# Kernel tuning notes

Measured on AMD Instinct MI355X. Metric: run time of the kernel, lower is better.

Reference implementation:

```python
import jax, jax.numpy as jnp
import numpy as np

B, PS, ENC = 64, 14, 2048
DEC, ATT, EMB = 512, 512, 512
V, L = 10000, 52


def setup_inputs() -> dict:
    key = jax.random.key(0)
    ks = jax.random.split(key, 24)
    rn = lambda k, shp, s=0.02: (jax.random.normal(k, shp) * s).astype(jnp.float32)
    lengths = jax.random.randint(ks[2], (B, 1), 2, L + 1)
    lengths = lengths.at[0, 0].set(L)  # ensure max(decode_lengths) == L-1 (static)
    return {
        "encoder_output": jax.random.normal(ks[0], (B, PS, PS, ENC), jnp.float32),
        "encoded_captions": jax.random.randint(ks[1], (B, L), 0, V),
        "caption_lengths": lengths,
        # embedding (torch init: uniform(-0.1, 0.1))
        "emb_W": jax.random.uniform(ks[3], (V, EMB), jnp.float32, -0.1, 0.1),
        # attention linears
        "att_enc_W": rn(ks[4], (ENC, ATT)), "att_enc_b": jnp.zeros((ATT,), jnp.float32),
        "att_dec_W": rn(ks[5], (DEC, ATT)), "att_dec_b": jnp.zeros((ATT,), jnp.float32),
        "att_full_w": rn(ks[6], (ATT,)), "att_full_b": jnp.zeros((), jnp.float32),
        # LSTMCell(input = EMB + ENC, hidden = DEC)
        "lstm_Wih": rn(ks[7], (4 * DEC, EMB + ENC)), "lstm_Whh": rn(ks[8], (4 * DEC, DEC)),
        "lstm_bih": jnp.zeros((4 * DEC,), jnp.float32), "lstm_bhh": jnp.zeros((4 * DEC,), jnp.float32),
        # init_h / init_c / f_beta / fc
        "initH_W": rn(ks[9], (ENC, DEC)), "initH_b": jnp.zeros((DEC,), jnp.float32),
        "initC_W": rn(ks[10], (ENC, DEC)), "initC_b": jnp.zeros((DEC,), jnp.float32),
        "fbeta_W": rn(ks[11], (DEC, ENC)), "fbeta_b": jnp.zeros((ENC,), jnp.float32),
        "fc_W": jax.random.uniform(ks[12], (DEC, V), jnp.float32, -0.1, 0.1),
        "fc_b": jnp.zeros((V,), jnp.float32),
    }


def reference(encoder_output, encoded_captions, caption_lengths,
              emb_W, att_enc_W, att_enc_b, att_dec_W, att_dec_b,
              att_full_w, att_full_b, lstm_Wih, lstm_Whh, lstm_bih, lstm_bhh,
              initH_W, initH_b, initC_W, initC_b, fbeta_W, fbeta_b, fc_W, fc_b):
    b = encoder_output.shape[0]
    lengths = caption_lengths[:, 0]
    order = jnp.argsort(-lengths)                     # sort descending (sort_idx)
    lengths = lengths[order]
    enc = encoder_output.reshape(b, -1, ENC)[order]   # [B, P, ENC]
    caps = encoded_captions[order]                    # [B, L]
    emb = emb_W[caps]                                 # [B, L, EMB]
    dec_len = lengths - 1                             # decode lengths
    T = caps.shape[1] - 1                             # static max(decode_lengths)

    mean_enc = enc.mean(axis=1)
    h0 = mean_enc @ initH_W + initH_b
    c0 = mean_enc @ initC_W + initC_b
    # precompute encoder half of the attention MLP once
    att1 = jnp.einsum('bpe,ea->bpa', enc, att_enc_W) + att_enc_b  # [B, P, ATT]

    def step(carry, t):
        h, c = carry
        mask = (t < dec_len)[:, None]                 # rows still decoding
        att2 = h @ att_dec_W + att_dec_b              # [B, ATT]
        e = jax.nn.relu(att1 + att2[:, None, :]) @ att_full_w + att_full_b  # [B, P]
        alpha = jax.nn.softmax(e, axis=-1)
        awe = jnp.einsum('bp,bpe->be', alpha, enc)    # attention-weighted encoding
        gate = jax.nn.sigmoid(h @ fbeta_W + fbeta_b)
        x = jnp.concatenate([emb[:, t, :], gate * awe], axis=1)
        gates = x @ lstm_Wih.T + lstm_bih + h @ lstm_Whh.T + lstm_bhh
        i, f, g, o = jnp.split(gates, 4, axis=1)
        c_new = jax.nn.sigmoid(f) * c + jax.nn.sigmoid(i) * jnp.tanh(g)
        h_new = jax.nn.sigmoid(o) * jnp.tanh(c_new)
        pred = h_new @ fc_W + fc_b                    # dropout p=0 -> identity
        h = jnp.where(mask, h_new, h)
        c = jnp.where(mask, c_new, c)
        return (h, c), (jnp.where(mask, pred, 0.0), jnp.where(mask, alpha, 0.0))

    _, (preds, alphas) = jax.lax.scan(step, (h0, c0), jnp.arange(T))
    preds = jnp.transpose(preds, (1, 0, 2))           # [B, T, V]
    alphas = jnp.transpose(alphas, (1, 0, 2))         # [B, T, P]
    return preds, caps, dec_len, alphas, order
```

## Files before the change

### kernel.cpp

```cpp
#include <hip/hip_runtime.h>
#include <hip/hip_cooperative_groups.h>
#include <math.h>

namespace cg = cooperative_groups;

#define BATCH 64
#define PIX   196
#define ENCD  2048
#define DECD  512
#define ATTD  512
#define EMBD  512
#define VOC   10000
#define LCAP  52
#define TSTEPS 51
#define XHDIM 3072

typedef __bf16 bfv8 __attribute__((ext_vector_type(8)));
typedef float  fv4  __attribute__((ext_vector_type(4)));

__device__ __forceinline__ float bf2f(unsigned short u) {
    union { unsigned int i; float f; } x; x.i = ((unsigned int)u) << 16; return x.f;
}
__device__ __forceinline__ unsigned short f2bf(float f) {
    union { float f; unsigned int i; } x; x.f = f;
    unsigned int r = x.i + 0x7fffu + ((x.i >> 16) & 1u);
    return (unsigned short)(r >> 16);
}

__global__ void k_setup(const int* caps, const int* lens,
                        int* order, int* declen,
                        float* caps_out, float* declen_out, float* order_out) {
    __shared__ int sl[64];
    __shared__ int so[64];
    int tid = threadIdx.x;
    sl[tid] = lens[tid];
    __syncthreads();
    int li = sl[tid];
    int pos = 0;
    for (int j = 0; j < 64; ++j) {
        int lj = sl[j];
        if (lj > li || (lj == li && j < tid)) pos++;
    }
    so[pos] = tid;
    __syncthreads();
    int ob = so[tid];
    order[tid] = ob;
    int dl = sl[ob] - 1;
    declen[tid] = dl;
    order_out[tid] = (float)ob;
    declen_out[tid] = (float)dl;
    for (int l = 0; l < LCAP; ++l)
        caps_out[tid * LCAP + l] = (float)caps[ob * LCAP + l];
}

__global__ void k_emb_all(const float* embW, const int* caps, const int* order,
                          unsigned short* emb_all, unsigned short* xh) {
    int b = blockIdx.x, t = blockIdx.y, tid = threadIdx.x;
    int tok = caps[order[b] * LCAP + t];
    float4 v = *(const float4*)(embW + (size_t)tok * EMBD + tid * 4);
    ushort4 o;
    o.x = f2bf(v.x); o.y = f2bf(v.y); o.z = f2bf(v.z); o.w = f2bf(v.w);
    *(ushort4*)(emb_all + ((size_t)t * 64 + b) * EMBD + tid * 4) = o;
    if (t == 0)
        *(ushort4*)(xh + (size_t)b * XHDIM + tid * 4) = o;
}

__global__ __launch_bounds__(256) void k_cvt_T(const float* src, unsigned short* dst,
                                               int R, int C) {
    __shared__ float tile[64][65];
    int c0 = blockIdx.x * 64, r0 = blockIdx.y * 64, tid = threadIdx.x;
    for (int idx = tid; idx < 4096; idx += 256) {
        int r = idx >> 6, c = idx & 63;
        float v = 0.f;
        if (r0 + r < R && c0 + c < C) v = src[(size_t)(r0 + r) * C + c0 + c];
        tile[r][c] = v;
    }
    __syncthreads();
    for (int idx = tid; idx < 4096; idx += 256) {
        int c = idx >> 6, r = idx & 63;
        if (c0 + c < C && r0 + r < R)
            dst[(size_t)(c0 + c) * R + r0 + r] = f2bf(tile[r][c]);
    }
}

__global__ void k_cvt_comb(const float* Wih, const float* Whh, unsigned short* W) {
    int j = blockIdx.x, tid = threadIdx.x;
    for (int k = tid * 4; k < XHDIM; k += 1024) {
        const float* src = (k < 2560) ? (Wih + (size_t)j * 2560 + k)
                                      : (Whh + (size_t)j * 512 + (k - 2560));
        float4 v = *(const float4*)src;
        ushort4 o;
        o.x = f2bf(v.x); o.y = f2bf(v.y); o.z = f2bf(v.z); o.w = f2bf(v.w);
        *(ushort4*)(W + (size_t)j * XHDIM + k) = o;
    }
}

__global__ void k_cvt_enc(const float* enc, const int* order, unsigned short* enc_bf) {
    int b = blockIdx.x, p = blockIdx.y, tid = threadIdx.x;
    const float* src = enc + ((size_t)order[b] * PIX + p) * ENCD + tid * 8;
    float4 v0 = *(const float4*)src;
    float4 v1 = *(const float4*)(src + 4);
    unsigned short o[8];
    o[0] = f2bf(v0.x); o[1] = f2bf(v0.y); o[2] = f2bf(v0.z); o[3] = f2bf(v0.w);
    o[4] = f2bf(v1.x); o[5] = f2bf(v1.y); o[6] = f2bf(v1.z); o[7] = f2bf(v1.w);
    *(uint4*)(enc_bf + ((size_t)b * PIX + p) * ENCD + tid * 8) = *(uint4*)o;
}

__global__ void k_mean(const float* enc, const int* order, float* meanv) {
    int b = blockIdx.x;
    int col = blockIdx.y * 256 + threadIdx.x;
    int ob = order[b];
    const float* base = enc + (size_t)ob * PIX * ENCD + col;
    float acc = 0.f;
    for (int p = 0; p < PIX; ++p) acc += base[(size_t)p * ENCD];
    meanv[b * ENCD + col] = acc * (1.0f / (float)PIX);
}

__global__ __launch_bounds__(256) void k_h0c0(const float* meanv,
                                              const float* WH, const float* bH,
                                              const float* WC, const float* bC,
                                              float* h, float* c, unsigned short* xh) {
    __shared__ float As[64 * 33];
    __shared__ float Bs[32 * 65];
    int nt = blockIdx.x, tid = threadIdx.x;
    const float* W; const float* bias; float* out; int j0; bool isH;
    if (nt < 8) { W = WH; bias = bH; out = h; j0 = nt * 64; isH = true; }
    else        { W = WC; bias = bC; out = c; j0 = (nt - 8) * 64; isH = false; }
    float acc[4][4] = {};
    int tr = tid & 15, tc = tid >> 4;
    for (int k0 = 0; k0 < ENCD; k0 += 32) {
        for (int idx = tid; idx < 512; idx += 256) {
            int rl = idx >> 3, k4 = (idx & 7) << 2;
            float4 v = *(const float4*)(meanv + (size_t)rl * ENCD + k0 + k4);
            float* d = As + rl * 33 + k4;
            d[0] = v.x; d[1] = v.y; d[2] = v.z; d[3] = v.w;
        }
        for (int idx = tid; idx < 512; idx += 256) {
            int k = idx >> 4, j4 = (idx & 15) << 2;
            float4 v = *(const float4*)(W + (size_t)(k0 + k) * DECD + j0 + j4);
            float* d = Bs + k * 65 + j4;
            d[0] = v.x; d[1] = v.y; d[2] = v.z; d[3] = v.w;
        }
        __syncthreads();
        for (int kk = 0; kk < 32; ++kk) {
            float a[4], bb[4];
            for (int i = 0; i < 4; ++i) a[i] = As[(tr * 4 + i) * 33 + kk];
            for (int i = 0; i < 4; ++i) bb[i] = Bs[kk * 65 + tc * 4 + i];
            for (int i = 0; i < 4; ++i)
                for (int j2 = 0; j2 < 4; ++j2) acc[i][j2] += a[i] * bb[j2];
        }
        __syncthreads();
    }
    for (int i = 0; i < 4; ++i)
        for (int j2 = 0; j2 < 4; ++j2) {
            int r = tr * 4 + i, j = j0 + tc * 4 + j2;
            float v = acc[i][j2] + bias[j];
            out[r * DECD + j] = v;
            if (isH) xh[(size_t)r * XHDIM + 2560 + j] = f2bf(v);
        }
}

__device__ __forceinline__ void mm64_core(
    const unsigned short* __restrict__ A, int lda,
    const unsigned short* __restrict__ Bt, int ldb,
    int K, int nvalid,
    unsigned short* __restrict__ As, unsigned short* __restrict__ Bs,
    fv4* __restrict__ acc)
{
    const int tid = threadIdx.x;
    const int lane = tid & 63;
    const int w = tid >> 6, wr = w >> 1, wc = w & 1;
    const int lr = lane & 15, lk = (lane >> 4) << 3;
    const int sr = tid >> 2, sc = (tid & 3) << 3;
    const unsigned short* ap = A + (size_t)sr * lda + sc;
    const unsigned short* bp = Bt + (size_t)sr * ldb + sc;
    const bool bok = sr < nvalid;
    unsigned short* aw = As + sr * 40 + sc;
    unsigned short* bw = Bs + sr * 40 + sc;
    const unsigned short* a0p = As + (wr * 32 + lr) * 40 + lk;
    const unsigned short* a1p = a0p + 16 * 40;
    const unsigned short* b0p = Bs + (wc * 32 + lr) * 40 + lk;
    const unsigned short* b1p = b0p + 16 * 40;

    uint4 av = *(const uint4*)ap;
    uint4 bv;
    if (bok) bv = *(const uint4*)bp; else { bv.x = bv.y = bv.z = bv.w = 0u; }

    for (int k0 = 0; k0 < K; k0 += 32) {
        __syncthreads();
        *(uint4*)aw = av;
        *(uint4*)bw = bv;
        if (k0 + 32 < K) {
            av = *(const uint4*)(ap + k0 + 32);
            if (bok) bv = *(const uint4*)(bp + k0 + 32);
            else { bv.x = bv.y = bv.z = bv.w = 0u; }
        }
        __syncthreads();
        bfv8 a0 = *(const bfv8*)a0p;
        bfv8 a1 = *(const bfv8*)a1p;
        bfv8 b0 = *(const bfv8*)b0p;
        bfv8 b1 = *(const bfv8*)b1p;
        acc[0] = __builtin_amdgcn_mfma_f32_16x16x32_bf16(a0, b0, acc[0], 0, 0, 0);
        acc[1] = __builtin_amdgcn_mfma_f32_16x16x32_bf16(a0, b1, acc[1], 0, 0, 0);
        acc[2] = __builtin_amdgcn_mfma_f32_16x16x32_bf16(a1, b0, acc[2], 0, 0, 0);
        acc[3] = __builtin_amdgcn_mfma_f32_16x16x32_bf16(a1, b1, acc[3], 0, 0, 0);
    }
}

#define MM64_DECL_EPI \
    int lane = threadIdx.x & 63; int w = threadIdx.x >> 6; \
    int wr = w >> 1, wc = w & 1; \
    int rg = (lane >> 4) << 2, cg = lane & 15;

__global__ __launch_bounds__(256) void k_att1_mfma(
    const unsigned short* __restrict__ enc_bf, const unsigned short* __restrict__ WaeT,
    const float* __restrict__ bias, unsigned short* __restrict__ att1bf) {
    __shared__ __align__(16) unsigned short As[64 * 40];
    __shared__ __align__(16) unsigned short Bs[64 * 40];
    int r0 = blockIdx.x * 64, a0 = blockIdx.y * 64;
    fv4 acc[4];
    acc[0] = (fv4)0.f; acc[1] = (fv4)0.f; acc[2] = (fv4)0.f; acc[3] = (fv4)0.f;
    mm64_core(enc_bf + (size_t)r0 * ENCD, ENCD,
              WaeT + (size_t)a0 * ENCD, ENCD, ENCD, 64, As, Bs, acc);
    MM64_DECL_EPI
    #pragma unroll
    for (int m = 0; m < 2; ++m)
      #pragma unroll
      for (int n = 0; n < 2; ++n)
        #pragma unroll
        for (int r = 0; r < 4; ++r) {
            int row = r0 + wr * 32 + m * 16 + rg + r;
            int col = a0 + wc * 32 + n * 16 + cg;
            att1bf[(size_t)row * ATTD + col] = f2bf(acc[m * 2 + n][r] + bias[col]);
        }
}

__global__ __launch_bounds__(256) void k_fc_mfma(
    const unsigned short* __restrict__ hallbf, const unsigned short* __restrict__ WfcT,
    const float* __restrict__ bias, const int* __restrict__ declen,
    float* __restrict__ preds) {
    __shared__ __align__(16) unsigned short As[64 * 40];
    __shared__ __align__(16) unsigned short Bs[64 * 40];
    int v0 = blockIdx.x * 64, tt = blockIdx.y;
    int nv = VOC - v0; if (nv > 64) nv = 64;
    fv4 acc[4];
    acc[0] = (fv4)0.f; acc[1] = (fv4)0.f; acc[2] = (fv4)0.f; acc[3] = (fv4)0.f;
    mm64_core(hallbf + (size_t)tt * 64 * DECD, DECD,
              WfcT + (size_t)v0 * DECD, DECD, DECD, nv, As, Bs, acc);
    MM64_DECL_EPI
    #pragma unroll
    for (int m = 0; m < 2; ++m)
      #pragma unroll
      for (int n = 0; n < 2; ++n)
        #pragma unroll
        for (int r = 0; r < 4; ++r) {
            int b = wr * 32 + m * 16 + rg + r;
            int v = v0 + wc * 32 + n * 16 + cg;
            if (v < VOC) {
                bool mask = tt < declen[b];
                preds[((size_t)b * TSTEPS + tt) * VOC + v] =
                    mask ? (acc[m * 2 + n][r] + bias[v]) : 0.f;
            }
        }
}

struct LoopArgs {
    const unsigned short* W2T;
    const unsigned short* Wcomb;
    const unsigned short* att1;
    const unsigned short* enc;
    const unsigned short* emb_all;
    unsigned short* xh;
    unsigned short* hall;
    const float* bad; const float* bfb;
    const float* wfull; const float* bfull;
    const float* bih; const float* bhh;
    float* att2; float* gate; float* e; float* part;
    float* h; float* c; float* alphas;
    const int* declen;
};

__global__ __launch_bounds__(256) void k_loop(LoopArgs a) {
    cg::grid_group grid = cg::this_grid();
    __shared__ __align__(16) unsigned short As[64 * 40];
    __shared__ __align__(16) unsigned short Bs[64 * 40];
    __shared__ float sal[256];
    __shared__ float sred[256];
    __shared__ float sacc[2048];
    const int bid = blockIdx.x, tid = threadIdx.x;

    for (int t = 0; t < TSTEPS; ++t) {
        if (bid < 40) {
            int j0 = bid * 64;
            fv4 acc[4];
            acc[0] = (fv4)0.f; acc[1] = (fv4)0.f; acc[2] = (fv4)0.f; acc[3] = (fv4)0.f;
            mm64_core(a.xh + 2560, XHDIM, a.W2T + (size_t)j0 * DECD, DECD,
                      DECD, 64, As, Bs, acc);
            MM64_DECL_EPI
            #pragma unroll
            for (int m = 0; m < 2; ++m)
              #pragma unroll
              for (int n = 0; n < 2; ++n)
                #pragma unroll
                for (int r = 0; r < 4; ++r) {
                    int row = wr * 32 + m * 16 + rg + r;
                    int jg = j0 + wc * 32 + n * 16 + cg;
                    float v = acc[m * 2 + n][r];
                    if (jg < ATTD) {
                        a.att2[row * ATTD + jg] = v + a.bad[jg];
                    } else {
                        int jj = jg - ATTD;
                        a.gate[row * ENCD + jj] = 1.f / (1.f + expf(-(v + a.bfb[jj])));
                    }
                }
        } else if (bid < 72) {
            int jt = bid - 40;
            fv4 acc[4];
            acc[0] = (fv4)0.f; acc[1] = (fv4)0.f; acc[2] = (fv4)0.f; acc[3] = (fv4)0.f;
            mm64_core(a.xh + 2560, XHDIM,
                      a.Wcomb + (size_t)jt * 64 * XHDIM + 2560, XHDIM,
                      512, 64, As, Bs, acc);
            float* out = a.part + (size_t)5 * (64 * 2048);
            MM64_DECL_EPI
            #pragma unroll
            for (int m = 0; m < 2; ++m)
              #pragma unroll
              for (int n = 0; n < 2; ++n)
                #pragma unroll
                for (int r = 0; r < 4; ++r) {
                    int row = wr * 32 + m * 16 + rg + r;
                    int col = jt * 64 + wc * 32 + n * 16 + cg;
                    out[row * 2048 + col] = acc[m * 2 + n][r];
                }
        }
        grid.sync();

        {
            int lane = tid & 63;
            int gw = bid * 4 + (tid >> 6);
            const float* a2base = a.att2;
            for (int u = gw; u < BATCH * PIX; u += 1024) {
                int b = u / PIX, p = u % PIX;
                uint4 v = *(const uint4*)(a.att1 + ((size_t)b * PIX + p) * ATTD + lane * 8);
                const unsigned short* us = (const unsigned short*)&v;
                const float* a2 = a2base + b * ATTD + lane * 8;
                float4 a2a = *(const float4*)a2;
                float4 a2b = *(const float4*)(a2 + 4);
                const float* wf = a.wfull + lane * 8;
                float4 wfa = *(const float4*)wf;
                float4 wfb = *(const float4*)(wf + 4);
                float accv;
                accv  = fmaxf(bf2f(us[0]) + a2a.x, 0.f) * wfa.x;
                accv += fmaxf(bf2f(us[1]) + a2a.y, 0.f) * wfa.y;
                accv += fmaxf(bf2f(us[2]) + a2a.z, 0.f) * wfa.z;
                accv += fmaxf(bf2f(us[3]) + a2a.w, 0.f) * wfa.w;
                accv += fmaxf(bf2f(us[4]) + a2b.x, 0.f) * wfb.x;
                accv += fmaxf(bf2f(us[5]) + a2b.y, 0.f) * wfb.y;
                accv += fmaxf(bf2f(us[6]) + a2b.z, 0.f) * wfb.z;
                accv += fmaxf(bf2f(us[7]) + a2b.w, 0.f) * wfb.w;
                for (int off = 32; off; off >>= 1) accv += __shfl_down(accv, off);
                if (lane == 0) a.e[b * PIX + p] = accv + a.bfull[0];
            }
        }
        grid.sync();

        {
            int b = bid >> 2, pair = bid & 3;
            float ev = (tid < PIX) ? a.e[b * PIX + tid] : -1e30f;
            sred[tid] = ev; __syncthreads();
            for (int s = 128; s; s >>= 1) {
                if (tid < s) sred[tid] = fmaxf(sred[tid], sred[tid + s]);
                __syncthreads();
            }
            float m = sred[0]; __syncthreads();
            float pv = (tid < PIX) ? expf(ev - m) : 0.f;
            sred[tid] = pv; __syncthreads();
            for (int s = 128; s; s >>= 1) {
                if (tid < s) sred[tid] += sred[tid + s];
                __syncthreads();
            }
            float inv = 1.f / sred[0];
            float al = pv * inv;
            sal[tid] = al;
            if (pair == 0 && tid < PIX) {
                bool mask = t < a.declen[b];
                a.alphas[((size_t)b * TSTEPS + t) * PIX + tid] = mask ? al : 0.f;
            }
            __syncthreads();
            int g = tid & 31, pp = tid >> 5;
            #pragma unroll
            for (int cc = 0; cc < 2; ++cc) {
                int ch = pair * 2 + cc;
                float acc[8] = {};
                const unsigned short* base =
                    a.enc + (size_t)b * PIX * ENCD + ch * 256 + g * 8;
                for (int p = pp; p < PIX; p += 8) {
                    uint4 v = *(const uint4*)(base + (size_t)p * ENCD);
                    const unsigned short* us = (const unsigned short*)&v;
                    float av = sal[p];
                    #pragma unroll
                    for (int jj = 0; jj < 8; ++jj) acc[jj] += av * bf2f(us[jj]);
                }
                #pragma unroll
                for (int jj = 0; jj < 8; ++jj) sacc[pp * 256 + g * 8 + jj] = acc[jj];
                __syncthreads();
                float s = 0.f;
                #pragma unroll
                for (int q = 0; q < 8; ++q) s += sacc[q * 256 + tid];
                int col = ch * 256 + tid;
                a.xh[(size_t)b * XHDIM + EMBD + col] = f2bf(a.gate[b * ENCD + col] * s);
                __syncthreads();
            }
        }
        grid.sync();

        if (bid < 160) {
            int jt = bid / 5, kc = bid % 5;
            fv4 acc[4];
            acc[0] = (fv4)0.f; acc[1] = (fv4)0.f; acc[2] = (fv4)0.f; acc[3] = (fv4)0.f;
            mm64_core(a.xh + kc * 512, XHDIM,
                      a.Wcomb + (size_t)jt * 64 * XHDIM + kc * 512, XHDIM,
                      512, 64, As, Bs, acc);
            float* out = a.part + (size_t)kc * (64 * 2048);
            MM64_DECL_EPI
            #pragma unroll
            for (int m = 0; m < 2; ++m)
              #pragma unroll
              for (int n = 0; n < 2; ++n)
                #pragma unroll
                for (int r = 0; r < 4; ++r) {
                    int row = wr * 32 + m * 16 + rg + r;
                    int col = jt * 64 + wc * 32 + n * 16 + cg;
                    out[row * 2048 + col] = acc[m * 2 + n][r];
                }
        }
        grid.sync();

        if (bid < 128) {
            int b = bid >> 1, d = (bid & 1) * 256 + tid;
            float gv[4];
            #pragma unroll
            for (int q = 0; q < 4; ++q) {
                int j = q * 512 + d;
                float acc = a.bih[j] + a.bhh[j];
                #pragma unroll
                for (int kc = 0; kc < 6; ++kc)
                    acc += a.part[(size_t)kc * 131072 + b * 2048 + j];
                gv[q] = acc;
            }
            float si = 1.f / (1.f + expf(-gv[0]));
            float sf = 1.f / (1.f + expf(-gv[1]));
            float gg = tanhf(gv[2]);
            float so = 1.f / (1.f + expf(-gv[3]));
            float c_old = a.c[b * DECD + d], h_old = a.h[b * DECD + d];
            float c_new = sf * c_old + si * gg;
            float h_new = so * tanhf(c_new);
            bool mask = t < a.declen[b];
            float h_keep = mask ? h_new : h_old;
            a.h[b * DECD + d] = h_keep;
            a.c[b * DECD + d] = mask ? c_new : c_old;
            a.xh[(size_t)b * XHDIM + 2560 + d] = f2bf(h_keep);
            a.hall[((size_t)t * 64 + b) * DECD + d] = f2bf(h_new);
            if (t + 1 < TSTEPS)
                a.xh[(size_t)b * XHDIM + d] = a.emb_all[((size_t)(t + 1) * 64 + b) * EMBD + d];
        }
        grid.sync();
    }
}

__global__ __launch_bounds__(256) void k_att2gate_mfma(
    const unsigned short* __restrict__ xh, const unsigned short* __restrict__ W2T,
    const float* __restrict__ bad, const float* __restrict__ bfb,
    float* __restrict__ att2, float* __restrict__ gate) {
    __shared__ __align__(16) unsigned short As[64 * 40];
    __shared__ __align__(16) unsigned short Bs[64 * 40];
    int j0 = blockIdx.x * 64;
    fv4 acc[4];
    acc[0] = (fv4)0.f; acc[1] = (fv4)0.f; acc[2] = (fv4)0.f; acc[3] = (fv4)0.f;
    mm64_core(xh + 2560, XHDIM, W2T + (size_t)j0 * DECD, DECD, DECD, 64, As, Bs, acc);
    MM64_DECL_EPI
    for (int m = 0; m < 2; ++m)
      for (int n = 0; n < 2; ++n)
        for (int r = 0; r < 4; ++r) {
            int row = wr * 32 + m * 16 + rg + r;
            int jg = j0 + wc * 32 + n * 16 + cg;
            float v = acc[m * 2 + n][r];
            if (jg < ATTD) att2[row * ATTD + jg] = v + bad[jg];
            else { int jj = jg - ATTD; gate[row * ENCD + jj] = 1.f / (1.f + expf(-(v + bfb[jj]))); }
        }
}

__global__ __launch_bounds__(256) void k_gates_mfma(
    const unsigned short* __restrict__ xh, const unsigned short* __restrict__ W,
    float* __restrict__ partial) {
    __shared__ __align__(16) unsigned short As[64 * 40];
    __shared__ __align__(16) unsigned short Bs[64 * 40];
    int jt = blockIdx.x, kc = blockIdx.y;
    fv4 acc[4];
    acc[0] = (fv4)0.f; acc[1] = (fv4)0.f; acc[2] = (fv4)0.f; acc[3] = (fv4)0.f;
    mm64_core(xh + kc * 512, XHDIM,
              W + (size_t)jt * 64 * XHDIM + kc * 512, XHDIM, 512, 64, As, Bs, acc);
    float* out = partial + (size_t)kc * (64 * 2048);
    MM64_DECL_EPI
    for (int m = 0; m < 2; ++m)
      for (int n = 0; n < 2; ++n)
        for (int r = 0; r < 4; ++r) {
            int row = wr * 32 + m * 16 + rg + r;
            int col = jt * 64 + wc * 32 + n * 16 + cg;
            out[row * 2048 + col] = acc[m * 2 + n][r];
        }
}

__global__ void k_e(const unsigned short* att1bf, const float* att2,
                    const float* wfull, const float* bfull, float* e) {
    __shared__ float a2s[512];
    __shared__ float wfs[512];
    int b = blockIdx.x, tid = threadIdx.x;
    a2s[tid] = att2[b * ATTD + tid];
    a2s[tid + 256] = att2[b * ATTD + tid + 256];
    wfs[tid] = wfull[tid];
    wfs[tid + 256] = wfull[tid + 256];
    __syncthreads();
    int p = blockIdx.y * 4 + (tid >> 6);
    int lane = tid & 63;
    uint4 v = *(const uint4*)(att1bf + ((size_t)b * PIX + p) * ATTD + lane * 8);
    const unsigned short* us = (const unsigned short*)&v;
    float acc = 0.f;
    for (int jj = 0; jj < 8; ++jj) {
        int a = lane * 8 + jj;
        float x = bf2f(us[jj]) + a2s[a];
        x = fmaxf(x, 0.f);
        acc += x * wfs[a];
    }
    for (int off = 32; off; off >>= 1) acc += __shfl_down(acc, off);
    if (lane == 0) e[b * PIX + p] = acc + bfull[0];
}

__global__ void k_awe(const float* e, const unsigned short* enc_bf,
                      const float* gate, const int* declen,
                      unsigned short* xh, float* alphas_out, int t) {
    __shared__ float sal[256];
    __shared__ float sred[256];
    __shared__ float sacc[2048];
    int b = blockIdx.x, ch = blockIdx.y, tid = threadIdx.x;
    float ev = (tid < PIX) ? e[b * PIX + tid] : -1e30f;
    sred[tid] = ev; __syncthreads();
    for (int s = 128; s; s >>= 1) { if (tid < s) sred[tid] = fmaxf(sred[tid], sred[tid + s]); __syncthreads(); }
    float m = sred[0]; __syncthreads();
    float pv = (tid < PIX) ? expf(ev - m) : 0.f;
    sred[tid] = pv; __syncthreads();
    for (int s = 128; s; s >>= 1) { if (tid < s) sred[tid] += sred[tid + s]; __syncthreads(); }
    float inv = 1.f / sred[0];
    float al = pv * inv;
    sal[tid] = al;
    if (ch == 0 && tid < PIX) {
        bool mask = t < declen[b];
        alphas_out[((size_t)b * TSTEPS + t) * PIX + tid] = mask ? al : 0.f;
    }
    __syncthreads();
    int g = tid & 31, pp = tid >> 5;
    float acc[8] = {};
    const unsigned short* base = enc_bf + (size_t)b * PIX * ENCD + ch * 256 + g * 8;
    for (int p = pp; p < PIX; p += 8) {
        uint4 v = *(const uint4*)(base + (size_t)p * ENCD);
        const unsigned short* us = (const unsigned short*)&v;
        float a = sal[p];
        for (int jj = 0; jj < 8; ++jj) acc[jj] += a * bf2f(us[jj]);
    }
    for (int jj = 0; jj < 8; ++jj) sacc[pp * 256 + g * 8 + jj] = acc[jj];
    __syncthreads();
    float s = 0.f;
    for (int q = 0; q < 8; ++q) s += sacc[q * 256 + tid];
    int col = ch * 256 + tid;
    xh[(size_t)b * XHDIM + EMBD + col] = f2bf(gate[b * ENCD + col] * s);
}

__global__ void k_update(const float* partial, const float* bih, const float* bhh,
                         const int* declen, float* h, float* c,
                         unsigned short* hallbf, const unsigned short* emb_all,
                         unsigned short* xh, int t) {
    int b = blockIdx.x, d = threadIdx.x;
    float g[4];
    for (int q = 0; q < 4; ++q) {
        int j = q * 512 + d;
        float acc = bih[j] + bhh[j];
        for (int kc = 0; kc < 6; ++kc) acc += partial[(size_t)kc * 131072 + b * 2048 + j];
        g[q] = acc;
    }
    float si = 1.f / (1.f + expf(-g[0]));
    float sf = 1.f / (1.f + expf(-g[1]));
    float gg = tanhf(g[2]);
    float so = 1.f / (1.f + expf(-g[3]));
    float c_old = c[b * DECD + d], h_old = h[b * DECD + d];
    float c_new = sf * c_old + si * gg;
    float h_new = so * tanhf(c_new);
    bool mask = t < declen[b];
    float h_keep = mask ? h_new : h_old;
    h[b * DECD + d] = h_keep;
    c[b * DECD + d] = mask ? c_new : c_old;
    xh[(size_t)b * XHDIM + 2560 + d] = f2bf(h_keep);
    hallbf[((size_t)t * 64 + b) * DECD + d] = f2bf(h_new);
    if (t + 1 < TSTEPS)
        xh[(size_t)b * XHDIM + d] = emb_all[((size_t)(t + 1) * 64 + b) * EMBD + d];
}

extern "C" void kernel_launch(void* const* d_in, const int* in_sizes, int n_in,
                              void* d_out, int out_size, void* d_ws, size_t ws_size,
                              hipStream_t stream) {
    const float* enc      = (const float*)d_in[0];
    const int*   caps     = (const int*)d_in[1];
    const int*   lens     = (const int*)d_in[2];
    const float* embW     = (const float*)d_in[3];
    const float* att_enc_W = (const float*)d_in[4];
    const float* att_enc_b = (const float*)d_in[5];
    const float* att_dec_W = (const float*)d_in[6];
    const float* att_dec_b = (const float*)d_in[7];
    const float* att_full_w = (const float*)d_in[8];
    const float* att_full_b = (const float*)d_in[9];
    const float* lstm_Wih = (const float*)d_in[10];
    const float* lstm_Whh = (const float*)d_in[11];
    const float* lstm_bih = (const float*)d_in[12];
    const float* lstm_bhh = (const float*)d_in[13];
    const float* initH_W  = (const float*)d_in[14];
    const float* initH_b  = (const float*)d_in[15];
    const float* initC_W  = (const float*)d_in[16];
    const float* initC_b  = (const float*)d_in[17];
    const float* fbeta_W  = (const float*)d_in[18];
    const float* fbeta_b  = (const float*)d_in[19];
    const float* fc_W     = (const float*)d_in[20];
    const float* fc_b     = (const float*)d_in[21];

    float* o = (float*)d_out;
    float* preds_out  = o;
    float* caps_out   = o + (size_t)BATCH * TSTEPS * VOC;
    float* declen_out = caps_out + (size_t)BATCH * LCAP;
    float* order_out  = declen_out + BATCH;
    float* alphas_out = order_out + BATCH;

    char* wsb = (char*)d_ws;
    int* i_order  = (int*)wsb;
    int* i_declen = i_order + 64;
    float* f = (float*)(wsb + 512);
    float* f_h     = f;  f += (size_t)BATCH * DECD;
    float* f_c     = f;  f += (size_t)BATCH * DECD;
    float* f_att2  = f;  f += (size_t)BATCH * ATTD;
    float* f_gate  = f;  f += (size_t)BATCH * ENCD;
    float* f_e     = f;  f += (size_t)BATCH * PIX;
    f = (float*)(((uintptr_t)f + 255) & ~(uintptr_t)255);
    float* f_part  = f;  f += (size_t)6 * BATCH * 2048;
    float* f_mean = f_part;
    unsigned short* WaeT = (unsigned short*)(f_part + (size_t)BATCH * ENCD);
    f = (float*)(((uintptr_t)f + 255) & ~(uintptr_t)255);
    unsigned short* bf = (unsigned short*)f;
    unsigned short* xh_bf    = bf;  bf += (size_t)BATCH * XHDIM;
    unsigned short* att1_bf  = bf;  bf += (size_t)BATCH * PIX * ATTD;
    unsigned short* Wcomb_bf = bf;  bf += (size_t)2048 * XHDIM;
    unsigned short* W2T      = bf;  bf += (size_t)(ATTD + ENCD) * DECD;
    unsigned short* WfcT     = bf;  bf += (size_t)VOC * DECD;
    unsigned short* emb_all  = bf;  bf += (size_t)TSTEPS * BATCH * EMBD;
    unsigned short* hall_bf  = bf;  bf += (size_t)TSTEPS * BATCH * DECD;
    bf = (unsigned short*)(((uintptr_t)bf + 255) & ~(uintptr_t)255);
    unsigned short* enc_bf   = bf;  bf += (size_t)BATCH * PIX * ENCD;

    k_setup<<<1, 64, 0, stream>>>(caps, lens, i_order, i_declen,
                                  caps_out, declen_out, order_out);
    k_emb_all<<<dim3(BATCH, TSTEPS), 128, 0, stream>>>(embW, caps, i_order,
                                                       emb_all, xh_bf);
    k_cvt_comb<<<2048, 256, 0, stream>>>(lstm_Wih, lstm_Whh, Wcomb_bf);
    k_cvt_enc<<<dim3(BATCH, PIX), 256, 0, stream>>>(enc, i_order, enc_bf);
    k_cvt_T<<<dim3(8, 8),   256, 0, stream>>>(att_dec_W, W2T, DECD, ATTD);
    k_cvt_T<<<dim3(32, 8),  256, 0, stream>>>(fbeta_W, W2T + (size_t)ATTD * DECD, DECD, ENCD);
    k_cvt_T<<<dim3(8, 32),  256, 0, stream>>>(att_enc_W, WaeT, ENCD, ATTD);
    k_cvt_T<<<dim3(157, 8), 256, 0, stream>>>(fc_W, WfcT, DECD, VOC);
    k_mean<<<dim3(BATCH, ENCD / 256), 256, 0, stream>>>(enc, i_order, f_mean);
    k_h0c0<<<16, 256, 0, stream>>>(f_mean, initH_W, initH_b, initC_W, initC_b,
                                   f_h, f_c, xh_bf);
    k_att1_mfma<<<dim3(PIX, ATTD / 64), 256, 0, stream>>>(enc_bf, WaeT,
                                                          att_enc_b, att1_bf);

    int maxb = 0;
    hipError_t qerr = hipOccupancyMaxActiveBlocksPerMultiprocessor(
        &maxb, (const void*)k_loop, 256, 0);
    bool coop_ok = (qerr == hipSuccess) && (maxb >= 1);

    if (coop_ok) {
        LoopArgs la;
        la.W2T = W2T; la.Wcomb = Wcomb_bf; la.att1 = att1_bf; la.enc = enc_bf;
        la.emb_all = emb_all; la.xh = xh_bf; la.hall = hall_bf;
        la.bad = att_dec_b; la.bfb = fbeta_b; la.wfull = att_full_w;
        la.bfull = att_full_b; la.bih = lstm_bih; la.bhh = lstm_bhh;
        la.att2 = f_att2; la.gate = f_gate; la.e = f_e; la.part = f_part;
        la.h = f_h; la.c = f_c; la.alphas = alphas_out; la.declen = i_declen;
        void* kargs[] = { (void*)&la };
        hipError_t lerr = hipLaunchCooperativeKernel(
            (const void*)k_loop, dim3(256), dim3(256), kargs, 0, stream);
        coop_ok = (lerr == hipSuccess);
    }

    if (!coop_ok) {
        for (int t = 0; t < TSTEPS; ++t) {
            k_att2gate_mfma<<<40, 256, 0, stream>>>(xh_bf, W2T, att_dec_b, fbeta_b,
                                                    f_att2, f_gate);
            k_e<<<dim3(BATCH, 49), 256, 0, stream>>>(att1_bf, f_att2, att_full_w,
                                                     att_full_b, f_e);
            k_awe<<<dim3(BATCH, 8), 256, 0, stream>>>(f_e, enc_bf, f_gate, i_declen,
                                                      xh_bf, alphas_out, t);
            k_gates_mfma<<<dim3(32, 6), 256, 0, stream>>>(xh_bf, Wcomb_bf, f_part);
            k_update<<<BATCH, DECD, 0, stream>>>(f_part, lstm_bih, lstm_bhh, i_declen,
                                                 f_h, f_c, hall_bf, emb_all, xh_bf, t);
        }
    }

    k_fc_mfma<<<dim3((VOC + 63) / 64, TSTEPS), 256, 0, stream>>>(hall_bf, WfcT,
                                                                 fc_b, i_declen,
                                                                 preds_out);
}
```

Before: 2.705 ms.

## Cut grid syncs per step and overlap fc projection inside persistent loop

Permutes the LSTM weight rows so that each 64-column gate tile holds the i,f,g,o gates for 16 hidden units. The gate GEMM can then run over the full K range in one block per tile and apply the LSTM cell update in its epilogue, which removes the split-K partial buffers and a separate update phase. The attention score and softmax phases are merged per batch row in shared memory, which drops another grid barrier. The fc vocabulary projection for step t-1 now runs on otherwise idle blocks during step t instead of as a separate trailing kernel. In exchange, each gate tile does a longer serial K loop (2560) on only 32 blocks, and shared memory use per block grows.

```diff
diff --git a/kernel.cpp b/kernel.cpp
--- a/kernel.cpp
+++ b/kernel.cpp
@@ -85,13 +85,15 @@
 
 __global__ void k_cvt_comb(const float* Wih, const float* Whh, unsigned short* W) {
     int j = blockIdx.x, tid = threadIdx.x;
+    int q = j >> 9, d = j & 511;
+    int nr = ((d >> 4) << 6) + (q << 4) + (d & 15);
     for (int k = tid * 4; k < XHDIM; k += 1024) {
         const float* src = (k < 2560) ? (Wih + (size_t)j * 2560 + k)
                                       : (Whh + (size_t)j * 512 + (k - 2560));
         float4 v = *(const float4*)src;
         ushort4 o;
         o.x = f2bf(v.x); o.y = f2bf(v.y); o.z = f2bf(v.z); o.w = f2bf(v.w);
-        *(ushort4*)(W + (size_t)j * XHDIM + k) = o;
+        *(ushort4*)(W + (size_t)nr * XHDIM + k) = o;
     }
 }
 
@@ -235,13 +237,12 @@
         }
 }
 
-__global__ __launch_bounds__(256) void k_fc_mfma(
+__device__ __forceinline__ void fc_tile(
     const unsigned short* __restrict__ hallbf, const unsigned short* __restrict__ WfcT,
     const float* __restrict__ bias, const int* __restrict__ declen,
-    float* __restrict__ preds) {
-    __shared__ __align__(16) unsigned short As[64 * 40];
-    __shared__ __align__(16) unsigned short Bs[64 * 40];
-    int v0 = blockIdx.x * 64, tt = blockIdx.y;
+    float* __restrict__ preds, int vt, int tt,
+    unsigned short* __restrict__ As, unsigned short* __restrict__ Bs) {
+    int v0 = vt * 64;
     int nv = VOC - v0; if (nv > 64) nv = 64;
     fv4 acc[4];
     acc[0] = (fv4)0.f; acc[1] = (fv4)0.f; acc[2] = (fv4)0.f; acc[3] = (fv4)0.f;
@@ -264,19 +265,30 @@
         }
 }
 
+__global__ __launch_bounds__(256) void k_fc_mfma(
+    const unsigned short* __restrict__ hallbf, const unsigned short* __restrict__ WfcT,
+    const float* __restrict__ bias, const int* __restrict__ declen,
+    float* __restrict__ preds) {
+    __shared__ __align__(16) unsigned short As[64 * 40];
+    __shared__ __align__(16) unsigned short Bs[64 * 40];
+    fc_tile(hallbf, WfcT, bias, declen, preds, blockIdx.x, blockIdx.y, As, Bs);
+}
+
 struct LoopArgs {
     const unsigned short* W2T;
     const unsigned short* Wcomb;
     const unsigned short* att1;
     const unsigned short* enc;
     const unsigned short* emb_all;
+    const unsigned short* WfcT;
     unsigned short* xh;
     unsigned short* hall;
     const float* bad; const float* bfb;
     const float* wfull; const float* bfull;
     const float* bih; const float* bhh;
-    float* att2; float* gate; float* e; float* part;
-    float* h; float* c; float* alphas;
+    const float* fcb;
+    float* att2; float* gate; float* part5;
+    float* h; float* c; float* alphas; float* preds;
     const int* declen;
 };
 
@@ -287,6 +299,7 @@
     __shared__ float sal[256];
     __shared__ float sred[256];
     __shared__ float sacc[2048];
+    __shared__ float gacc[64][65];
     const int bid = blockIdx.x, tid = threadIdx.x;
 
     for (int t = 0; t < TSTEPS; ++t) {
@@ -320,7 +333,6 @@
             mm64_core(a.xh + 2560, XHDIM,
                       a.Wcomb + (size_t)jt * 64 * XHDIM + 2560, XHDIM,
                       512, 64, As, Bs, acc);
-            float* out = a.part + (size_t)5 * (64 * 2048);
             MM64_DECL_EPI
             #pragma unroll
             for (int m = 0; m < 2; ++m)
@@ -330,25 +342,24 @@
                 for (int r = 0; r < 4; ++r) {
                     int row = wr * 32 + m * 16 + rg + r;
                     int col = jt * 64 + wc * 32 + n * 16 + cg;
-                    out[row * 2048 + col] = acc[m * 2 + n][r];
+                    a.part5[row * 2048 + col] = acc[m * 2 + n][r];
                 }
         }
         grid.sync();
 
         {
-            int lane = tid & 63;
-            int gw = bid * 4 + (tid >> 6);
-            const float* a2base = a.att2;
-            for (int u = gw; u < BATCH * PIX; u += 1024) {
-                int b = u / PIX, p = u % PIX;
+            int b = bid >> 2, pair = bid & 3;
+            int lane = tid & 63, wv = tid >> 6;
+            const float* a2 = a.att2 + b * ATTD + lane * 8;
+            float4 a2a = *(const float4*)a2;
+            float4 a2b = *(const float4*)(a2 + 4);
+            const float* wf = a.wfull + lane * 8;
+            float4 wfa = *(const float4*)wf;
+            float4 wfb = *(const float4*)(wf + 4);
+            float bf0 = a.bfull[0];
+            for (int p = wv; p < PIX; p += 4) {
                 uint4 v = *(const uint4*)(a.att1 + ((size_t)b * PIX + p) * ATTD + lane * 8);
                 const unsigned short* us = (const unsigned short*)&v;
-                const float* a2 = a2base + b * ATTD + lane * 8;
-                float4 a2a = *(const float4*)a2;
-                float4 a2b = *(const float4*)(a2 + 4);
-                const float* wf = a.wfull + lane * 8;
-                float4 wfa = *(const float4*)wf;
-                float4 wfb = *(const float4*)(wf + 4);
                 float accv;
                 accv  = fmaxf(bf2f(us[0]) + a2a.x, 0.f) * wfa.x;
                 accv += fmaxf(bf2f(us[1]) + a2a.y, 0.f) * wfa.y;
@@ -359,14 +370,10 @@
                 accv += fmaxf(bf2f(us[6]) + a2b.z, 0.f) * wfb.z;
                 accv += fmaxf(bf2f(us[7]) + a2b.w, 0.f) * wfb.w;
                 for (int off = 32; off; off >>= 1) accv += __shfl_down(accv, off);
-                if (lane == 0) a.e[b * PIX + p] = accv + a.bfull[0];
+                if (lane == 0) sacc[p] = accv + bf0;
             }
-        }
-        grid.sync();
-
-        {
-            int b = bid >> 2, pair = bid & 3;
-            float ev = (tid < PIX) ? a.e[b * PIX + tid] : -1e30f;
+            __syncthreads();
+            float ev = (tid < PIX) ? sacc[tid] : -1e30f;
             sred[tid] = ev; __syncthreads();
             for (int s = 128; s; s >>= 1) {
                 if (tid < s) sred[tid] = fmaxf(sred[tid], sred[tid + s]);
@@ -386,6 +393,10 @@
                 bool mask = t < a.declen[b];
                 a.alphas[((size_t)b * TSTEPS + t) * PIX + tid] = mask ? al : 0.f;
             }
+            if (tid < 16)
+                *(uint4*)(a.xh + (size_t)b * XHDIM + pair * 128 + tid * 8) =
+                    *(const uint4*)(a.emb_all + ((size_t)t * 64 + b) * EMBD +
+                                    pair * 128 + tid * 8);
             __syncthreads();
             int g = tid & 31, pp = tid >> 5;
             #pragma unroll
@@ -414,58 +425,60 @@
         }
         grid.sync();
 
-        if (bid < 160) {
-            int jt = bid / 5, kc = bid % 5;
+        if (bid < 32) {
+            int jt = bid;
             fv4 acc[4];
             acc[0] = (fv4)0.f; acc[1] = (fv4)0.f; acc[2] = (fv4)0.f; acc[3] = (fv4)0.f;
-            mm64_core(a.xh + kc * 512, XHDIM,
-                      a.Wcomb + (size_t)jt * 64 * XHDIM + kc * 512, XHDIM,
-                      512, 64, As, Bs, acc);
-            float* out = a.part + (size_t)kc * (64 * 2048);
-            MM64_DECL_EPI
+            mm64_core(a.xh, XHDIM, a.Wcomb + (size_t)jt * 64 * XHDIM, XHDIM,
+                      2560, 64, As, Bs, acc);
+            {
+                MM64_DECL_EPI
+                #pragma unroll
+                for (int m = 0; m < 2; ++m)
+                  #pragma unroll
+                  for (int n = 0; n < 2; ++n)
+                    #pragma unroll
+                    for (int r = 0; r < 4; ++r)
+                        gacc[wr * 32 + m * 16 + rg + r][wc * 32 + n * 16 + cg] =
+                            acc[m * 2 + n][r];
+            }
+            __syncthreads();
             #pragma unroll
-            for (int m = 0; m < 2; ++m)
-              #pragma unroll
-              for (int n = 0; n < 2; ++n)
+            for (int it = 0; it < 4; ++it) {
+                int idx = it * 256 + tid;
+                int b = idx >> 4, dd = idx & 15;
+                int d = jt * 16 + dd;
+                float gv[4];
                 #pragma unroll
-                for (int r = 0; r < 4; ++r) {
-                    int row = wr * 32 + m * 16 + rg + r;
-                    int col = jt * 64 + wc * 32 + n * 16 + cg;
-                    out[row * 2048 + col] = acc[m * 2 + n][r];
+                for (int q = 0; q < 4; ++q) {
+                    int ccol = q * 16 + dd;
+                    gv[q] = gacc[b][ccol] + a.part5[b * 2048 + jt * 64 + ccol]
+                          + a.bih[q * 512 + d] + a.bhh[q * 512 + d];
                 }
+                float si = 1.f / (1.f + expf(-gv[0]));
+                float sf = 1.f / (1.f + expf(-gv[1]));
+                float gg = tanhf(gv[2]);
+                float so = 1.f / (1.f + expf(-gv[3]));
+                float c_old = a.c[b * DECD + d], h_old = a.h[b * DECD + d];
+                float c_new = sf * c_old + si * gg;
+                float h_new = so * tanhf(c_new);
+                bool mask = t < a.declen[b];
+                float h_keep = mask ? h_new : h_old;
+                a.h[b * DECD + d] = h_keep;
+                a.c[b * DECD + d] = mask ? c_new : c_old;
+                a.xh[(size_t)b * XHDIM + 2560 + d] = f2bf(h_keep);
+                a.hall[((size_t)t * 64 + b) * DECD + d] = f2bf(h_new);
+            }
+        } else if (bid < 189) {
+            if (t > 0)
+                fc_tile(a.hall, a.WfcT, a.fcb, a.declen, a.preds,
+                        bid - 32, t - 1, As, Bs);
         }
         grid.sync();
-
-        if (bid < 128) {
-            int b = bid >> 1, d = (bid & 1) * 256 + tid;
-            float gv[4];
-            #pragma unroll
-            for (int q = 0; q < 4; ++q) {
-                int j = q * 512 + d;
-                float acc = a.bih[j] + a.bhh[j];
-                #pragma unroll
-                for (int kc = 0; kc < 6; ++kc)
-                    acc += a.part[(size_t)kc * 131072 + b * 2048 + j];
-                gv[q] = acc;
-            }
-            float si = 1.f / (1.f + expf(-gv[0]));
-            float sf = 1.f / (1.f + expf(-gv[1]));
-            float gg = tanhf(gv[2]);
-            float so = 1.f / (1.f + expf(-gv[3]));
-            float c_old = a.c[b * DECD + d], h_old = a.h[b * DECD + d];
-            float c_new = sf * c_old + si * gg;
-            float h_new = so * tanhf(c_new);
-            bool mask = t < a.declen[b];
-            float h_keep = mask ? h_new : h_old;
-            a.h[b * DECD + d] = h_keep;
-            a.c[b * DECD + d] = mask ? c_new : c_old;
-            a.xh[(size_t)b * XHDIM + 2560 + d] = f2bf(h_keep);
-            a.hall[((size_t)t * 64 + b) * DECD + d] = f2bf(h_new);
-            if (t + 1 < TSTEPS)
-                a.xh[(size_t)b * XHDIM + d] = a.emb_all[((size_t)(t + 1) * 64 + b) * EMBD + d];
-        }
-        grid.sync();
-    }
+    }
+
+    if (bid < 157)
+        fc_tile(a.hall, a.WfcT, a.fcb, a.declen, a.preds, bid, TSTEPS - 1, As, Bs);
 }
 
 __global__ __launch_bounds__(256) void k_att2gate_mfma(
@@ -582,9 +595,9 @@
     int b = blockIdx.x, d = threadIdx.x;
     float g[4];
     for (int q = 0; q < 4; ++q) {
-        int j = q * 512 + d;
-        float acc = bih[j] + bhh[j];
-        for (int kc = 0; kc < 6; ++kc) acc += partial[(size_t)kc * 131072 + b * 2048 + j];
+        int ncol = ((d >> 4) << 6) + (q << 4) + (d & 15);
+        float acc = bih[q * 512 + d] + bhh[q * 512 + d];
+        for (int kc = 0; kc < 6; ++kc) acc += partial[(size_t)kc * 131072 + b * 2048 + ncol];
         g[q] = acc;
     }
     float si = 1.f / (1.f + expf(-g[0]));
@@ -686,11 +699,13 @@
     if (coop_ok) {
         LoopArgs la;
         la.W2T = W2T; la.Wcomb = Wcomb_bf; la.att1 = att1_bf; la.enc = enc_bf;
-        la.emb_all = emb_all; la.xh = xh_bf; la.hall = hall_bf;
+        la.emb_all = emb_all; la.WfcT = WfcT; la.xh = xh_bf; la.hall = hall_bf;
         la.bad = att_dec_b; la.bfb = fbeta_b; la.wfull = att_full_w;
         la.bfull = att_full_b; la.bih = lstm_bih; la.bhh = lstm_bhh;
-        la.att2 = f_att2; la.gate = f_gate; la.e = f_e; la.part = f_part;
-        la.h = f_h; la.c = f_c; la.alphas = alphas_out; la.declen = i_declen;
+        la.fcb = fc_b;
+        la.att2 = f_att2; la.gate = f_gate; la.part5 = f_part;
+        la.h = f_h; la.c = f_c; la.alphas = alphas_out; la.preds = preds_out;
+        la.declen = i_declen;
         void* kargs[] = { (void*)&la };
         hipError_t lerr = hipLaunchCooperativeKernel(
             (const void*)k_loop, dim3(256), dim3(256), kargs, 0, stream);
@@ -709,9 +724,8 @@
             k_update<<<BATCH, DECD, 0, stream>>>(f_part, lstm_bih, lstm_bhh, i_declen,
                                                  f_h, f_c, hall_bf, emb_all, xh_bf, t);
         }
-    }
-
-    k_fc_mfma<<<dim3((VOC + 63) / 64, TSTEPS), 256, 0, stream>>>(hall_bf, WfcT,
-                                                                 fc_b, i_declen,
-                                                                 preds_out);
-}
+        k_fc_mfma<<<dim3((VOC + 63) / 64, TSTEPS), 256, 0, stream>>>(hall_bf, WfcT,
+                                                                     fc_b, i_declen,
+                                                                     preds_out);
+    }
+}
```

Measured after the change: 2.708 ms. No clear change (+0.1%).
